# Kernel tuning notes

Measured on AMD Instinct MI355X. Metric: run time of the kernel, lower is better.

Reference implementation:

```python
import jax, jax.numpy as jnp
import numpy as np

D_MODEL = 1024
N_HEAD = 16


def setup_inputs() -> dict:
    key = jax.random.key(0)
    ks = jax.random.split(key, 12)
    B, L, D = 4, 2048, D_MODEL
    s = 1.0 / np.sqrt(D)
    inp = {
        'q': jax.random.normal(ks[0], (B, L, D), jnp.float32),
        'k': jax.random.normal(ks[1], (B, L, D), jnp.float32),
        'v': jax.random.normal(ks[2], (B, L, D), jnp.float32),
        'w_q': jax.random.normal(ks[3], (D, D), jnp.float32) * s,
        'b_q': jnp.zeros((D,), jnp.float32),
        'w_k': jax.random.normal(ks[4], (D, D), jnp.float32) * s,
        'b_k': jnp.zeros((D,), jnp.float32),
        'w_v': jax.random.normal(ks[5], (D, D), jnp.float32) * s,
        'b_v': jnp.zeros((D,), jnp.float32),
        'w_o': jax.random.normal(ks[6], (D, D), jnp.float32) * s,
        'b_o': jnp.zeros((D,), jnp.float32),
    }
    return inp


def _split(t, n_head):
    B, L, D = t.shape
    return t.reshape(B, L, n_head, D // n_head).transpose(0, 2, 1, 3)  # [B,H,L,d]


def reference(q, k, v, w_q, b_q, w_k, b_k, w_v, b_v, w_o, b_o):
    # linear projections (torch Linear: x @ W^T + b)
    qp = q @ w_q.T + b_q
    kp = k @ w_k.T + b_k
    vp = v @ w_v.T + b_v
    qh, kh, vh = _split(qp, N_HEAD), _split(kp, N_HEAD), _split(vp, N_HEAD)
    d_head = qh.shape[-1]
    score = jnp.einsum('bhqd,bhkd->bhqk', qh, kh) / jnp.sqrt(jnp.float32(d_head))
    attn = jax.nn.softmax(score, axis=-1)
    out = jnp.einsum('bhqk,bhkd->bhqd', attn, vh)  # [B,H,L,d]
    B, H, L, d = out.shape
    out = out.transpose(0, 2, 1, 3).reshape(B, L, H * d)
    return out @ w_o.T + b_o
```

## Files before the change

### kernel.cpp

```cpp
#include <hip/hip_runtime.h>
#include <hip/hip_bf16.h>
#include <cstdint>
#include <cstddef>

#define D_MODEL 1024
#define N_HEAD  16
#define DH      64
#define SEQ     2048
#define BATCH   4

typedef __attribute__((ext_vector_type(8))) __bf16 bf16x8;
typedef __attribute__((ext_vector_type(8))) unsigned short u16x8;
typedef __attribute__((ext_vector_type(4))) unsigned short u16x4;
typedef __attribute__((ext_vector_type(4))) float f32x4;

#define AS3 __attribute__((address_space(3)))

static __device__ __forceinline__ unsigned short f2bf(float f) {
  unsigned int u = __builtin_bit_cast(unsigned int, f);
  u += 0x7fffu + ((u >> 16) & 1u);
  return (unsigned short)(u >> 16);
}

static __device__ __forceinline__ float fexp2(float x) {
#if __has_builtin(__builtin_amdgcn_exp2f)
  return __builtin_amdgcn_exp2f(x);
#else
  return exp2f(x);
#endif
}

static __device__ __forceinline__ void gll16(const unsigned short* g, unsigned short* l) {
  __builtin_amdgcn_global_load_lds((const __attribute__((address_space(1))) void*)g,
                                   (AS3 void*)l, 16, 0, 0);
}

static __device__ __forceinline__ int xcd_swz(int bid, int nwg) {
  const int cpx = nwg >> 3;
  return (bid & 7) * cpx + (bid >> 3);
}

__global__ void cvtk(const float* __restrict__ in, unsigned short* __restrict__ out, int n) {
  int stride = gridDim.x * blockDim.x;
  for (int i = blockIdx.x * blockDim.x + threadIdx.x; i * 8 < n; i += stride) {
    float4 a = *(const float4*)(in + (size_t)i * 8);
    float4 b = *(const float4*)(in + (size_t)i * 8 + 4);
    u16x8 o;
    o[0] = f2bf(a.x); o[1] = f2bf(a.y); o[2] = f2bf(a.z); o[3] = f2bf(a.w);
    o[4] = f2bf(b.x); o[5] = f2bf(b.y); o[6] = f2bf(b.z); o[7] = f2bf(b.w);
    *(u16x8*)(out + (size_t)i * 8) = o;
  }
}

template<int OUTF32>
__global__ __launch_bounds__(256) void gemm_bt(
    const unsigned short* __restrict__ A,
    const unsigned short* __restrict__ B,
    const float* __restrict__ bias,
    unsigned short* __restrict__ Cb, float* __restrict__ Cf,
    int M, int N, int K)
{
  alignas(16) __shared__ unsigned short As[2][128 * 32];
  alignas(16) __shared__ unsigned short Bs[2][128 * 32];
  const int t  = threadIdx.x;
  const int w  = t >> 6, l = t & 63;
  const int lr = l & 15, lk = l >> 4;

  const int nbx = N >> 7;
  const int swz = xcd_swz(blockIdx.x, gridDim.x);
  const int bn0 = (swz % nbx) * 128, bm0 = (swz / nbx) * 128;
  const int wm = (w >> 1) * 64, wn = (w & 1) * 64;

  f32x4 acc[4][4] = {};
  const int NT = K >> 5;

  auto stage = [&](int kt) {
    const int buf = kt & 1;
    const int k0 = kt << 5;
#pragma unroll
    for (int i = 0; i < 2; ++i) {
      int c = i * 256 + t;
      int row = c >> 2, ko = (c & 3) << 3;
      int ub = __builtin_amdgcn_readfirstlane((c & ~63) * 8);
      gll16(A + (size_t)(bm0 + row) * K + k0 + ko, &As[buf][ub]);
      gll16(B + (size_t)(bn0 + row) * K + k0 + ko, &Bs[buf][ub]);
    }
  };

  stage(0);
  asm volatile("s_waitcnt vmcnt(0)" ::: "memory");
  __syncthreads();

  for (int kt = 0; kt < NT; ++kt) {
    const int cur = kt & 1;
    stage((kt + 1) & (NT - 1));
    bf16x8 af[4], bfr[4];
#pragma unroll
    for (int i = 0; i < 4; ++i) {
      af[i]  = __builtin_bit_cast(bf16x8, *(const u16x8*)&As[cur][(wm + i * 16 + lr) * 32 + lk * 8]);
      bfr[i] = __builtin_bit_cast(bf16x8, *(const u16x8*)&Bs[cur][(wn + i * 16 + lr) * 32 + lk * 8]);
    }
#pragma unroll
    for (int mi = 0; mi < 4; ++mi)
#pragma unroll
      for (int ni = 0; ni < 4; ++ni)
        acc[mi][ni] = __builtin_amdgcn_mfma_f32_16x16x32_bf16(af[mi], bfr[ni], acc[mi][ni], 0, 0, 0);
    asm volatile("s_waitcnt vmcnt(0)" ::: "memory");
    __syncthreads();
  }

  float bv[4];
#pragma unroll
  for (int ni = 0; ni < 4; ++ni) bv[ni] = bias[bn0 + wn + ni * 16 + lr];
#pragma unroll
  for (int mi = 0; mi < 4; ++mi)
#pragma unroll
    for (int ni = 0; ni < 4; ++ni) {
      const int col = bn0 + wn + ni * 16 + lr;
#pragma unroll
      for (int r = 0; r < 4; ++r) {
        const int row = bm0 + wm + mi * 16 + lk * 4 + r;
        float v = acc[mi][ni][r] + bv[ni];
        if (OUTF32) Cf[(size_t)row * N + col] = v;
        else        Cb[(size_t)row * N + col] = f2bf(v);
      }
    }
}

__global__ __launch_bounds__(256) void attn_fwd(
    const unsigned short* __restrict__ Qp,
    const unsigned short* __restrict__ Kp,
    const unsigned short* __restrict__ Vp,
    unsigned short* __restrict__ Ao)
{
  alignas(16) __shared__ unsigned short Ks[2][64 * 64];
  alignas(16) __shared__ unsigned short Vt[2][64 * 64];
  alignas(16) __shared__ unsigned short Ps[4][32 * 64];

  const int t = threadIdx.x, w = t >> 6, l = t & 63;
  const int lr = l & 15, lk = l >> 4;
  const int swz = xcd_swz(blockIdx.x, gridDim.x);
  const int qt = swz & 15, h = (swz >> 4) & 15, b = swz >> 8;
  const int hoff = h * DH;
  const int q0 = qt * 128 + w * 32;

  bf16x8 qf[2][2];
#pragma unroll
  for (int mi = 0; mi < 2; ++mi)
#pragma unroll
    for (int kk = 0; kk < 2; ++kk)
      qf[mi][kk] = __builtin_bit_cast(bf16x8,
        *(const u16x8*)(Qp + (size_t)(b * SEQ + q0 + mi * 16 + lr) * D_MODEL + hoff + kk * 32 + lk * 8));

  f32x4 acc[2][4] = {};
  float m2[2]   = {-1e30f, -1e30f};
  float lrun[2] = {0.f, 0.f};
  const float C1  = 0.18033688f;
  const float THR = 11.541560f;

  auto stageK = [&](int jt) {
    const int buf = jt & 1;
    const size_t rbase = (size_t)b * SEQ + (size_t)jt * 64;
#pragma unroll
    for (int i = 0; i < 2; ++i) {
      const int c = i * 256 + t;
      const int ub = __builtin_amdgcn_readfirstlane((c & ~63) * 8);
      const int j = c >> 3, d = 8 * ((c & 7) ^ (j & 7));
      gll16(Kp + (rbase + j) * D_MODEL + hoff + d, &Ks[buf][ub]);
    }
  };
  u16x8 vreg[2];
  auto loadV = [&](int jt) {
    const size_t rbase = (size_t)b * SEQ + (size_t)jt * 64;
#pragma unroll
    for (int i = 0; i < 2; ++i) {
      const int cc = i * 256 + t;
      vreg[i] = *(const u16x8*)(Vp + (rbase + (cc >> 3)) * D_MODEL + hoff + (cc & 7) * 8);
    }
  };
  auto writeV = [&](int buf) {
#pragma unroll
    for (int i = 0; i < 2; ++i) {
      const int cc = i * 256 + t;
      const int j = cc >> 3, x = cc & 7;
#pragma unroll
      for (int m = 0; m < 8; ++m) {
        const int d = 8 * x + m;
        Vt[buf][d * 64 + 8 * ((j >> 3) ^ m ^ x) + (j & 7)] = vreg[i][m];
      }
    }
  };

  stageK(0);
  loadV(0);
  asm volatile("s_waitcnt vmcnt(0)" ::: "memory");
  writeV(0);
  __syncthreads();

  for (int jt = 0; jt < SEQ / 64; ++jt) {
    const int cur = jt & 1;
    const int nxt = (jt + 1) & (SEQ / 64 - 1);
    stageK(nxt);
    loadV(nxt);

    bf16x8 kb[4][2];
#pragma unroll
    for (int ni = 0; ni < 4; ++ni)
#pragma unroll
      for (int kk = 0; kk < 2; ++kk) {
        const int j = ni * 16 + lr;
        const int off = j * 64 + 8 * ((4 * kk + lk) ^ (j & 7));
        kb[ni][kk] = __builtin_bit_cast(bf16x8, *(const u16x8*)&Ks[cur][off]);
      }

    f32x4 s[2][4];
#pragma unroll
    for (int mi = 0; mi < 2; ++mi)
#pragma unroll
      for (int ni = 0; ni < 4; ++ni) {
        f32x4 z = {};
        z = __builtin_amdgcn_mfma_f32_16x16x32_bf16(kb[ni][0], qf[mi][0], z, 0, 0, 0);
        z = __builtin_amdgcn_mfma_f32_16x16x32_bf16(kb[ni][1], qf[mi][1], z, 0, 0, 0);
        s[mi][ni] = z;
      }

#pragma unroll
    for (int mi = 0; mi < 2; ++mi) {
      float vmax = s[mi][0][0];
#pragma unroll
      for (int ni = 0; ni < 4; ++ni)
#pragma unroll
        for (int r = 0; r < 4; ++r) vmax = fmaxf(vmax, s[mi][ni][r]);
      vmax = fmaxf(vmax, __shfl_xor(vmax, 16));
      vmax = fmaxf(vmax, __shfl_xor(vmax, 32));
      const float sm2 = vmax * C1;
      if (!__all(sm2 - m2[mi] <= THR)) {
        const float mnew  = fmaxf(m2[mi], sm2);
        const float alpha = fexp2(m2[mi] - mnew);
        m2[mi] = mnew;
        lrun[mi] *= alpha;
#pragma unroll
        for (int r = 0; r < 4; ++r) {
          const float ar = __shfl(alpha, (l & 48) | (((l >> 4) & 3) << 2) | r);
#pragma unroll
          for (int f = 0; f < 4; ++f) acc[mi][f][r] *= ar;
        }
      }
      float sum = 0.f;
      u16x4 pk[4];
#pragma unroll
      for (int ni = 0; ni < 4; ++ni)
#pragma unroll
        for (int r = 0; r < 4; ++r) {
          const float p = fexp2(fmaf(s[mi][ni][r], C1, -m2[mi]));
          sum += p;
          pk[ni][r] = f2bf(p);
        }
      sum += __shfl_xor(sum, 16);
      sum += __shfl_xor(sum, 32);
      lrun[mi] += sum;
      const int q = mi * 16 + lr;
#pragma unroll
      for (int nj = 0; nj < 4; ++nj) {
        const int off = q * 64 + (((nj * 32 + lk * 8) ^ ((q & 7) << 4)) >> 1);
        *(u16x4*)&Ps[w][off] = pk[nj];
      }
    }

    bf16x8 pa[2][2];
#pragma unroll
    for (int mi = 0; mi < 2; ++mi)
#pragma unroll
      for (int kk = 0; kk < 2; ++kk) {
        const int q = mi * 16 + lr;
        const int off = q * 64 + 8 * ((4 * kk + lk) ^ (q & 7));
        pa[mi][kk] = __builtin_bit_cast(bf16x8, *(const u16x8*)&Ps[w][off]);
      }

    bf16x8 vb[4][2];
#pragma unroll
    for (int f = 0; f < 4; ++f)
#pragma unroll
      for (int kk = 0; kk < 2; ++kk) {
        const int d = 16 * f + lr;
        const int off = d * 64 + 8 * ((4 * kk + lk) ^ (lr & 7) ^ ((2 * f + (lr >> 3)) & 7));
        vb[f][kk] = __builtin_bit_cast(bf16x8, *(const u16x8*)&Vt[cur][off]);
      }

#pragma unroll
    for (int mi = 0; mi < 2; ++mi)
#pragma unroll
      for (int f = 0; f < 4; ++f) {
        acc[mi][f] = __builtin_amdgcn_mfma_f32_16x16x32_bf16(pa[mi][0], vb[f][0], acc[mi][f], 0, 0, 0);
        acc[mi][f] = __builtin_amdgcn_mfma_f32_16x16x32_bf16(pa[mi][1], vb[f][1], acc[mi][f], 0, 0, 0);
      }

    asm volatile("s_waitcnt vmcnt(0)" ::: "memory");
    writeV(cur ^ 1);
    __syncthreads();
  }

#pragma unroll
  for (int mi = 0; mi < 2; ++mi)
#pragma unroll
    for (int r = 0; r < 4; ++r) {
      const float lr_r = __shfl(lrun[mi], (l & 48) | (((l >> 4) & 3) << 2) | r);
      const float inv = 1.0f / lr_r;
      const int row = q0 + mi * 16 + (l >> 4) * 4 + r;
#pragma unroll
      for (int f = 0; f < 4; ++f)
        Ao[(size_t)(b * SEQ + row) * D_MODEL + hoff + f * 16 + lr] = f2bf(acc[mi][f][r] * inv);
    }
}

extern "C" void kernel_launch(void* const* d_in, const int* in_sizes, int n_in,
                              void* d_out, int out_size, void* d_ws, size_t ws_size,
                              hipStream_t stream) {
  const float* q  = (const float*)d_in[0];
  const float* k  = (const float*)d_in[1];
  const float* v  = (const float*)d_in[2];
  const float* wq = (const float*)d_in[3];
  const float* bq = (const float*)d_in[4];
  const float* wk = (const float*)d_in[5];
  const float* bk = (const float*)d_in[6];
  const float* wv = (const float*)d_in[7];
  const float* bv = (const float*)d_in[8];
  const float* wo = (const float*)d_in[9];
  const float* bo = (const float*)d_in[10];
  float* out = (float*)d_out;

  const int M = BATCH * SEQ;
  const int D = D_MODEL;
  const size_t nMD = (size_t)M * D;
  const size_t nDD = (size_t)D * D;

  unsigned short* ws = (unsigned short*)d_ws;
  unsigned short* xb = ws;
  unsigned short* qp = xb + nMD;
  unsigned short* kp = qp + nMD;
  unsigned short* vp = kp + nMD;
  unsigned short* wb = vp + nMD;
  unsigned short* ao = xb;

  dim3 gg(512);

  cvtk<<<256,  256, 0, stream>>>(wq, wb, (int)nDD);
  cvtk<<<2048, 256, 0, stream>>>(q,  xb, (int)nMD);
  gemm_bt<0><<<gg, 256, 0, stream>>>(xb, wb, bq, qp, nullptr, M, D, D);

  cvtk<<<256,  256, 0, stream>>>(wk, wb, (int)nDD);
  cvtk<<<2048, 256, 0, stream>>>(k,  xb, (int)nMD);
  gemm_bt<0><<<gg, 256, 0, stream>>>(xb, wb, bk, kp, nullptr, M, D, D);

  cvtk<<<256,  256, 0, stream>>>(wv, wb, (int)nDD);
  cvtk<<<2048, 256, 0, stream>>>(v,  xb, (int)nMD);
  gemm_bt<0><<<gg, 256, 0, stream>>>(xb, wb, bv, vp, nullptr, M, D, D);

  attn_fwd<<<dim3(1024), 256, 0, stream>>>(qp, kp, vp, ao);

  cvtk<<<256, 256, 0, stream>>>(wo, wb, (int)nDD);
  gemm_bt<1><<<gg, 256, 0, stream>>>(ao, wb, bo, nullptr, out, M, D, D);
}
```

Baseline: 439.0 us.

## Widen GEMM K-tile with swizzled LDS, merge conversion launches, tune attention softmax

After: 410.8 us. 6.4% less time.

```diff
diff --git a/kernel.cpp b/kernel.cpp
--- a/kernel.cpp
+++ b/kernel.cpp
@@ -12,6 +12,7 @@
 typedef __attribute__((ext_vector_type(8))) __bf16 bf16x8;
 typedef __attribute__((ext_vector_type(8))) unsigned short u16x8;
 typedef __attribute__((ext_vector_type(4))) unsigned short u16x4;
+typedef __attribute__((ext_vector_type(2))) unsigned int u32x2;
 typedef __attribute__((ext_vector_type(4))) float f32x4;
 
 #define AS3 __attribute__((address_space(3)))
@@ -40,16 +41,21 @@
   return (bid & 7) * cpx + (bid >> 3);
 }
 
-__global__ void cvtk(const float* __restrict__ in, unsigned short* __restrict__ out, int n) {
-  int stride = gridDim.x * blockDim.x;
-  for (int i = blockIdx.x * blockDim.x + threadIdx.x; i * 8 < n; i += stride) {
-    float4 a = *(const float4*)(in + (size_t)i * 8);
-    float4 b = *(const float4*)(in + (size_t)i * 8 + 4);
-    u16x8 o;
-    o[0] = f2bf(a.x); o[1] = f2bf(a.y); o[2] = f2bf(a.z); o[3] = f2bf(a.w);
-    o[4] = f2bf(b.x); o[5] = f2bf(b.y); o[6] = f2bf(b.z); o[7] = f2bf(b.w);
-    *(u16x8*)(out + (size_t)i * 8) = o;
-  }
+__global__ void cvtseg(const float* __restrict__ i0, unsigned short* __restrict__ o0, int nb0,
+                       const float* __restrict__ i1, unsigned short* __restrict__ o1, int nb1,
+                       const float* __restrict__ i2, unsigned short* __restrict__ o2) {
+  int bb = blockIdx.x;
+  const float* in; unsigned short* out;
+  if (bb < nb0)            { in = i0; out = o0; }
+  else if (bb < nb0 + nb1) { in = i1; out = o1; bb -= nb0; }
+  else                     { in = i2; out = o2; bb -= nb0 + nb1; }
+  const size_t base = (size_t)bb * 2048 + (size_t)threadIdx.x * 8;
+  float4 a = *(const float4*)(in + base);
+  float4 b = *(const float4*)(in + base + 4);
+  u16x8 o;
+  o[0] = f2bf(a.x); o[1] = f2bf(a.y); o[2] = f2bf(a.z); o[3] = f2bf(a.w);
+  o[4] = f2bf(b.x); o[5] = f2bf(b.y); o[6] = f2bf(b.z); o[7] = f2bf(b.w);
+  *(u16x8*)(out + base) = o;
 }
 
 template<int OUTF32>
@@ -60,8 +66,8 @@
     unsigned short* __restrict__ Cb, float* __restrict__ Cf,
     int M, int N, int K)
 {
-  alignas(16) __shared__ unsigned short As[2][128 * 32];
-  alignas(16) __shared__ unsigned short Bs[2][128 * 32];
+  alignas(16) __shared__ unsigned short As[2][128 * 64];
+  alignas(16) __shared__ unsigned short Bs[2][128 * 64];
   const int t  = threadIdx.x;
   const int w  = t >> 6, l = t & 63;
   const int lr = l & 15, lk = l >> 4;
@@ -72,15 +78,16 @@
   const int wm = (w >> 1) * 64, wn = (w & 1) * 64;
 
   f32x4 acc[4][4] = {};
-  const int NT = K >> 5;
+  const int NT = K >> 6;
 
   auto stage = [&](int kt) {
     const int buf = kt & 1;
-    const int k0 = kt << 5;
-#pragma unroll
-    for (int i = 0; i < 2; ++i) {
+    const int k0 = kt << 6;
+#pragma unroll
+    for (int i = 0; i < 4; ++i) {
       int c = i * 256 + t;
-      int row = c >> 2, ko = (c & 3) << 3;
+      int row = c >> 3, x = c & 7;
+      int ko = 8 * (x ^ (row & 7));
       int ub = __builtin_amdgcn_readfirstlane((c & ~63) * 8);
       gll16(A + (size_t)(bm0 + row) * K + k0 + ko, &As[buf][ub]);
       gll16(B + (size_t)(bn0 + row) * K + k0 + ko, &Bs[buf][ub]);
@@ -94,17 +101,24 @@
   for (int kt = 0; kt < NT; ++kt) {
     const int cur = kt & 1;
     stage((kt + 1) & (NT - 1));
-    bf16x8 af[4], bfr[4];
-#pragma unroll
-    for (int i = 0; i < 4; ++i) {
-      af[i]  = __builtin_bit_cast(bf16x8, *(const u16x8*)&As[cur][(wm + i * 16 + lr) * 32 + lk * 8]);
-      bfr[i] = __builtin_bit_cast(bf16x8, *(const u16x8*)&Bs[cur][(wn + i * 16 + lr) * 32 + lk * 8]);
-    }
-#pragma unroll
-    for (int mi = 0; mi < 4; ++mi)
-#pragma unroll
-      for (int ni = 0; ni < 4; ++ni)
-        acc[mi][ni] = __builtin_amdgcn_mfma_f32_16x16x32_bf16(af[mi], bfr[ni], acc[mi][ni], 0, 0, 0);
+    bf16x8 af[4][2], bfr[4][2];
+#pragma unroll
+    for (int i = 0; i < 4; ++i)
+#pragma unroll
+      for (int kk = 0; kk < 2; ++kk) {
+        const int ra = wm + i * 16 + lr, rb = wn + i * 16 + lr;
+        af[i][kk]  = __builtin_bit_cast(bf16x8,
+          *(const u16x8*)&As[cur][ra * 64 + 8 * ((4 * kk + lk) ^ (ra & 7))]);
+        bfr[i][kk] = __builtin_bit_cast(bf16x8,
+          *(const u16x8*)&Bs[cur][rb * 64 + 8 * ((4 * kk + lk) ^ (rb & 7))]);
+      }
+#pragma unroll
+    for (int kk = 0; kk < 2; ++kk)
+#pragma unroll
+      for (int mi = 0; mi < 4; ++mi)
+#pragma unroll
+        for (int ni = 0; ni < 4; ++ni)
+          acc[mi][ni] = __builtin_amdgcn_mfma_f32_16x16x32_bf16(af[mi][kk], bfr[ni][kk], acc[mi][ni], 0, 0, 0);
     asm volatile("s_waitcnt vmcnt(0)" ::: "memory");
     __syncthreads();
   }
@@ -214,6 +228,7 @@
       }
 
     f32x4 s[2][4];
+    __builtin_amdgcn_s_setprio(1);
 #pragma unroll
     for (int mi = 0; mi < 2; ++mi)
 #pragma unroll
@@ -223,6 +238,7 @@
         z = __builtin_amdgcn_mfma_f32_16x16x32_bf16(kb[ni][1], qf[mi][1], z, 0, 0, 0);
         s[mi][ni] = z;
       }
+    __builtin_amdgcn_s_setprio(0);
 
 #pragma unroll
     for (int mi = 0; mi < 2; ++mi) {
@@ -247,15 +263,17 @@
         }
       }
       float sum = 0.f;
-      u16x4 pk[4];
-#pragma unroll
-      for (int ni = 0; ni < 4; ++ni)
-#pragma unroll
-        for (int r = 0; r < 4; ++r) {
-          const float p = fexp2(fmaf(s[mi][ni][r], C1, -m2[mi]));
-          sum += p;
-          pk[ni][r] = f2bf(p);
-        }
+      unsigned int pw[4][2];
+#pragma unroll
+      for (int ni = 0; ni < 4; ++ni) {
+        float p0 = fexp2(fmaf(s[mi][ni][0], C1, -m2[mi]));
+        float p1 = fexp2(fmaf(s[mi][ni][1], C1, -m2[mi]));
+        float p2 = fexp2(fmaf(s[mi][ni][2], C1, -m2[mi]));
+        float p3 = fexp2(fmaf(s[mi][ni][3], C1, -m2[mi]));
+        sum += (p0 + p1) + (p2 + p3);
+        asm("v_cvt_pk_bf16_f32 %0, %1, %2" : "=v"(pw[ni][0]) : "v"(p0), "v"(p1));
+        asm("v_cvt_pk_bf16_f32 %0, %1, %2" : "=v"(pw[ni][1]) : "v"(p2), "v"(p3));
+      }
       sum += __shfl_xor(sum, 16);
       sum += __shfl_xor(sum, 32);
       lrun[mi] += sum;
@@ -263,7 +281,8 @@
 #pragma unroll
       for (int nj = 0; nj < 4; ++nj) {
         const int off = q * 64 + (((nj * 32 + lk * 8) ^ ((q & 7) << 4)) >> 1);
-        *(u16x4*)&Ps[w][off] = pk[nj];
+        u32x2 pv2 = {pw[nj][0], pw[nj][1]};
+        *(u32x2*)&Ps[w][off] = pv2;
       }
     }
 
@@ -287,6 +306,7 @@
         vb[f][kk] = __builtin_bit_cast(bf16x8, *(const u16x8*)&Vt[cur][off]);
       }
 
+    __builtin_amdgcn_s_setprio(1);
 #pragma unroll
     for (int mi = 0; mi < 2; ++mi)
 #pragma unroll
@@ -294,6 +314,7 @@
         acc[mi][f] = __builtin_amdgcn_mfma_f32_16x16x32_bf16(pa[mi][0], vb[f][0], acc[mi][f], 0, 0, 0);
         acc[mi][f] = __builtin_amdgcn_mfma_f32_16x16x32_bf16(pa[mi][1], vb[f][1], acc[mi][f], 0, 0, 0);
       }
+    __builtin_amdgcn_s_setprio(0);
 
     asm volatile("s_waitcnt vmcnt(0)" ::: "memory");
     writeV(cur ^ 1);
@@ -333,31 +354,30 @@
   const int D = D_MODEL;
   const size_t nMD = (size_t)M * D;
   const size_t nDD = (size_t)D * D;
-
-  unsigned short* ws = (unsigned short*)d_ws;
-  unsigned short* xb = ws;
-  unsigned short* qp = xb + nMD;
-  unsigned short* kp = qp + nMD;
-  unsigned short* vp = kp + nMD;
-  unsigned short* wb = vp + nMD;
-  unsigned short* ao = xb;
+  const int nbW = (int)(nDD / 2048);
+  const int nbX = (int)(nMD / 2048);
+
+  unsigned short* ws  = (unsigned short*)d_ws;
+  unsigned short* xb  = ws;
+  unsigned short* qp  = xb + nMD;
+  unsigned short* kp  = qp + nMD;
+  unsigned short* vp  = kp + nMD;
+  unsigned short* wb  = vp + nMD;
+  unsigned short* wob = wb + nDD;
+  unsigned short* ao  = xb;
 
   dim3 gg(512);
 
-  cvtk<<<256,  256, 0, stream>>>(wq, wb, (int)nDD);
-  cvtk<<<2048, 256, 0, stream>>>(q,  xb, (int)nMD);
+  cvtseg<<<nbW + nbX, 256, 0, stream>>>(wq, wb, nbW, q, xb, nbX, wq, wb);
   gemm_bt<0><<<gg, 256, 0, stream>>>(xb, wb, bq, qp, nullptr, M, D, D);
 
-  cvtk<<<256,  256, 0, stream>>>(wk, wb, (int)nDD);
-  cvtk<<<2048, 256, 0, stream>>>(k,  xb, (int)nMD);
+  cvtseg<<<nbW + nbX, 256, 0, stream>>>(wk, wb, nbW, k, xb, nbX, wk, wb);
   gemm_bt<0><<<gg, 256, 0, stream>>>(xb, wb, bk, kp, nullptr, M, D, D);
 
-  cvtk<<<256,  256, 0, stream>>>(wv, wb, (int)nDD);
-  cvtk<<<2048, 256, 0, stream>>>(v,  xb, (int)nMD);
+  cvtseg<<<nbW + nbX + nbW, 256, 0, stream>>>(wv, wb, nbW, v, xb, nbX, wo, wob);
   gemm_bt<0><<<gg, 256, 0, stream>>>(xb, wb, bv, vp, nullptr, M, D, D);
 
   attn_fwd<<<dim3(1024), 256, 0, stream>>>(qp, kp, vp, ao);
 
-  cvtk<<<256, 256, 0, stream>>>(wo, wb, (int)nDD);
-  gemm_bt<1><<<gg, 256, 0, stream>>>(ao, wb, bo, nullptr, out, M, D, D);
-}
+  gemm_bt<1><<<gg, 256, 0, stream>>>(ao, wob, bo, nullptr, out, M, D, D);
+}
```
